# Optimization experiments

Hardware: AMD Instinct MI355X
Metric: run time of the kernel (lower is better)

Reference implementation:

```python
import jax, jax.numpy as jnp
import numpy as np

EPS = 1e-5  # torch nn.LayerNorm default


def _ln(x, g, b):
    m = jnp.mean(x, axis=-1, keepdims=True)
    v = jnp.mean(jnp.square(x - m), axis=-1, keepdims=True)
    return (x - m) * jax.lax.rsqrt(v + EPS) * g + b


def setup_inputs() -> dict:
    key = jax.random.key(0)
    ks = jax.random.split(key, 21)
    B, D, H, O = 32768, 512, 256, 128
    E, T, NS, NT, G = 10, 3, 4, 2, 64

    def rn(k, shape, s=0.02):
        return jax.random.normal(k, shape, jnp.float32) * s

    return dict(
        x=jax.random.normal(ks[0], (B, D), jnp.float32),
        ew1=rn(ks[1], (E, D, H)), eb1=rn(ks[2], (E, H)),
        eg1=1.0 + rn(ks[3], (E, H), 0.1), ebt1=rn(ks[4], (E, H), 0.1),
        ew2=rn(ks[5], (E, H, H)), eb2=rn(ks[6], (E, H)),
        eg2=1.0 + rn(ks[7], (E, H), 0.1), ebt2=rn(ks[8], (E, H), 0.1),
        ew3=rn(ks[9], (E, H, O)), eb3=rn(ks[10], (E, O)),
        eg3=1.0 + rn(ks[11], (E, O), 0.1), ebt3=rn(ks[12], (E, O), 0.1),
        tg_w1=rn(ks[13], (T, D, G)), tg_b1=rn(ks[14], (T, G)),
        tg_w2=rn(ks[15], (T, G, NS + NT)), tg_b2=rn(ks[16], (T, NS + NT)),
        sg_w1=rn(ks[17], (D, G)), sg_b1=rn(ks[18], (G,)),
        sg_w2=rn(ks[19], (G, E)), sg_b2=rn(ks[20], (E,)),
    )


def reference(x, ew1, eb1, eg1, ebt1, ew2, eb2, eg2, ebt2,
              ew3, eb3, eg3, ebt3, tg_w1, tg_b1, tg_w2, tg_b2,
              sg_w1, sg_b1, sg_w2, sg_b2):
    NS, NT, T = 4, 2, 3  # num_shared_experts, num_task_experts, num_tasks
    # Batched expert MLPs (eval mode: dropout is identity). eo: [E, B, O]
    h = jax.nn.relu(_ln(jnp.einsum('bd,edh->ebh', x, ew1) + eb1[:, None, :],
                        eg1[:, None, :], ebt1[:, None, :]))
    h = jax.nn.relu(_ln(jnp.einsum('ebh,ehk->ebk', h, ew2) + eb2[:, None, :],
                        eg2[:, None, :], ebt2[:, None, :]))
    eo = jax.nn.relu(_ln(jnp.einsum('ebh,eho->ebo', h, ew3) + eb3[:, None, :],
                         eg3[:, None, :], ebt3[:, None, :]))
    E, B, O = eo.shape
    shared = eo[:NS]                              # [NS, B, O]
    task_eo = eo[NS:].reshape(T, NT, B, O)        # [T, NT, B, O]

    # Per-task gates: softmax over NS+NT experts. gw: [T, B, NS+NT]
    gh = jax.nn.relu(jnp.einsum('bd,tdg->tbg', x, tg_w1) + tg_b1[:, None, :])
    gw = jax.nn.softmax(jnp.einsum('tbg,tge->tbe', gh, tg_w2) + tg_b2[:, None, :],
                        axis=-1)
    # combined: [T, NS+NT, B, O] (shared first, matching torch.cat order)
    combined = jnp.concatenate(
        [jnp.broadcast_to(shared[None], (T, NS, B, O)), task_eo], axis=1)
    task_out = jnp.einsum('tbe,tebo->tbo', gw, combined)  # [T, B, O]

    # Shared gate over all E experts (order: shared, task0, task1, task2)
    sgh = jax.nn.relu(x @ sg_w1 + sg_b1)
    sgw = jax.nn.softmax(sgh @ sg_w2 + sg_b2, axis=-1)    # [B, E]
    shared_out = jnp.einsum('be,ebo->bo', sgw, eo)        # [B, O]

    # Pack (task_final_outputs list, shared_output) as one [T+1, B, O] array
    return jnp.concatenate([task_out, shared_out[None]], axis=0)
```

## Files before the change

### kernel.cpp

```cpp
#include <hip/hip_runtime.h>
#include <math.h>

typedef __attribute__((ext_vector_type(8))) _Float16 half8;
typedef __attribute__((ext_vector_type(8))) short short8;
typedef __attribute__((ext_vector_type(4))) float float4v;

static __device__ __forceinline__ unsigned short f2h(float f) {
  union { _Float16 h; unsigned short u; } c;
  c.h = (_Float16)f;
  return c.u;
}
static __device__ __forceinline__ float h2f(unsigned short u) {
  union { unsigned short u; _Float16 h; } c;
  c.u = u;
  return (float)c.h;
}

static __device__ __forceinline__ void gload16(const unsigned short* g,
                                               unsigned short* l) {
  __builtin_amdgcn_global_load_lds(
      (const __attribute__((address_space(1))) unsigned int*)g,
      (__attribute__((address_space(3))) unsigned int*)l, 16, 0, 0);
}

__global__ __launch_bounds__(256)
void split_pack(const float* __restrict__ src, unsigned short* __restrict__ dh,
                unsigned short* __restrict__ dl, int K, int N) {
  __shared__ float t[32][33];
  src += (size_t)blockIdx.z * K * N;
  const size_t tsz = (size_t)N * 32;
  const size_t tb = ((size_t)blockIdx.z * (K >> 5) + blockIdx.x) * tsz;
  const int k0 = blockIdx.x * 32, n0 = blockIdx.y * 32;
  const int tid = threadIdx.x;
  const int r = tid >> 3, c4 = (tid & 7) * 4;

  const float4 v = *(const float4*)(src + (size_t)(k0 + r) * N + n0 + c4);
  t[r][c4 + 0] = v.x; t[r][c4 + 1] = v.y; t[r][c4 + 2] = v.z; t[r][c4 + 3] = v.w;
  __syncthreads();

  const int sel = tid >> 7;
  const int rl = (tid >> 2) & 31;
  const int qq = tid & 3;
  short8 vv;
  #pragma unroll
  for (int j = 0; j < 8; ++j) {
    const float f = t[qq * 8 + j][rl];
    const unsigned short hb = f2h(f);
    ((unsigned short*)&vv)[j] = sel ? f2h(f - h2f(hb)) : hb;
  }
  unsigned short* dst = (sel ? dl : dh) + tb +
      (size_t)(n0 + rl) * 32 + (qq ^ ((rl >> 1) & 3)) * 8;
  *(short8*)dst = vv;
}

template<int N, int NT>
__device__ __forceinline__ void ln_store_f16(
    float4v (*acc)[4], int w, int m, int q,
    const float* __restrict__ bias, const float* __restrict__ gamma,
    const float* __restrict__ beta,
    unsigned short* __restrict__ dst, int dstride,
    float (*sumP)[4], float (*sqP)[4]) {
  constexpr int NW = N / 4;
  float cb[NT], cg[NT], cbt[NT];
  #pragma unroll
  for (int t = 0; t < NT; ++t) {
    const int col = w * NW + t * 16 + m;
    cb[t] = bias[col]; cg[t] = gamma[col]; cbt[t] = beta[col];
  }
  #pragma unroll
  for (int s = 0; s < 4; ++s)
    #pragma unroll
    for (int r = 0; r < 4; ++r) {
      float s1 = 0.f, s2 = 0.f;
      #pragma unroll
      for (int t = 0; t < NT; ++t) {
        const float v = acc[s][t][r] + cb[t];
        s1 += v; s2 += v * v;
      }
      #pragma unroll
      for (int off = 1; off < 16; off <<= 1) {
        s1 += __shfl_xor(s1, off, 16);
        s2 += __shfl_xor(s2, off, 16);
      }
      if (m == 0) {
        sumP[s * 16 + q * 4 + r][w] = s1;
        sqP[s * 16 + q * 4 + r][w] = s2;
      }
    }
  __syncthreads();
  #pragma unroll
  for (int s = 0; s < 4; ++s)
    #pragma unroll
    for (int r = 0; r < 4; ++r) {
      const int row = s * 16 + q * 4 + r;
      const float S1 = sumP[row][0] + sumP[row][1] + sumP[row][2] + sumP[row][3];
      const float S2 = sqP[row][0] + sqP[row][1] + sqP[row][2] + sqP[row][3];
      const float mean = S1 * (1.f / N);
      const float var = S2 * (1.f / N) - mean * mean;
      const float inv = rsqrtf(var + 1e-5f);
      #pragma unroll
      for (int t = 0; t < NT; ++t) {
        const float o =
            fmaxf((acc[s][t][r] + cb[t] - mean) * inv * cg[t] + cbt[t], 0.f);
        dst[row * dstride + w * NW + t * 16 + m] = f2h(o);
      }
    }
  __syncthreads();
}

__global__ __launch_bounds__(256, 2)
void expert_tower(const float* __restrict__ x,
                  const unsigned short* __restrict__ w1h,
                  const unsigned short* __restrict__ w1l,
                  const float* __restrict__ eb1, const float* __restrict__ eg1,
                  const float* __restrict__ ebt1,
                  const unsigned short* __restrict__ w2h,
                  const unsigned short* __restrict__ w2l,
                  const float* __restrict__ eb2, const float* __restrict__ eg2,
                  const float* __restrict__ ebt2,
                  const unsigned short* __restrict__ w3h,
                  const unsigned short* __restrict__ w3l,
                  const float* __restrict__ eb3, const float* __restrict__ eg3,
                  const float* __restrict__ ebt3,
                  unsigned short* __restrict__ eo, int B) {
  __shared__ __align__(16) unsigned short pool[40960];
  float (*sumP)[4] = (float (*)[4])(pool + 16384);
  float (*sqP)[4]  = (float (*)[4])(pool + 16896);
  unsigned short* hbuf = pool + 24064;

  const int tid = threadIdx.x;
  const int w = tid >> 6, lane = tid & 63, m = lane & 15, q = lane >> 4;
  const int qs8 = (q ^ ((m >> 1) & 3)) * 8;
  const int wb = w * 512;
  const int m0 = blockIdx.x * 64;
  const int e = blockIdx.y;
  const int arow = tid >> 2, ap = tid & 3;
  const int aswz = arow * 32 + (ap ^ ((arow >> 1) & 3)) * 8;

  eb1 += (size_t)e * 256; eg1 += (size_t)e * 256; ebt1 += (size_t)e * 256;
  eb2 += (size_t)e * 256; eg2 += (size_t)e * 256; ebt2 += (size_t)e * 256;
  eb3 += (size_t)e * 128; eg3 += (size_t)e * 128; ebt3 += (size_t)e * 128;

  float4v acc[4][4];

  #pragma unroll
  for (int s = 0; s < 4; ++s)
    #pragma unroll
    for (int t = 0; t < 4; ++t) acc[s][t] = (float4v){0.f, 0.f, 0.f, 0.f};

  const float* xrow = x + (size_t)(m0 + arow) * 512 + ap * 8;
  float4 f0 = *(const float4*)xrow;
  float4 f1 = *(const float4*)(xrow + 4);

  {
    const float fv[8] = {f0.x, f0.y, f0.z, f0.w, f1.x, f1.y, f1.z, f1.w};
    half8 ra, rla;
    #pragma unroll
    for (int j = 0; j < 8; ++j) {
      const _Float16 hb = (_Float16)fv[j];
      ra[j] = hb;
      rla[j] = (_Float16)(fv[j] - (float)hb);
    }
    *(half8*)(pool + aswz) = ra;
    *(half8*)(pool + 2048 + aswz) = rla;
    const size_t tb = ((size_t)(e * 16)) * 8192 + tid * 8;
    #pragma unroll
    for (int i = 0; i < 4; ++i) {
      gload16(w1h + tb + i * 2048, pool + 8192 + wb + i * 2048);
      gload16(w1l + tb + i * 2048, pool + 8192 + 8192 + wb + i * 2048);
    }
    __builtin_amdgcn_sched_barrier(0);
    f0 = *(const float4*)(xrow + 32);
    f1 = *(const float4*)(xrow + 36);
    __builtin_amdgcn_sched_barrier(0);
    asm volatile("s_waitcnt vmcnt(2) lgkmcnt(0)" ::: "memory");
    __builtin_amdgcn_sched_barrier(0);
    __builtin_amdgcn_s_barrier();
  }

  #pragma unroll 2
  for (int kt = 0; kt < 16; ++kt) {
    const int cur = kt & 1, nxt = cur ^ 1;
    if (kt < 15) {
      const float fv[8] = {f0.x, f0.y, f0.z, f0.w, f1.x, f1.y, f1.z, f1.w};
      half8 ra, rla;
      #pragma unroll
      for (int j = 0; j < 8; ++j) {
        const _Float16 hb = (_Float16)fv[j];
        ra[j] = hb;
        rla[j] = (_Float16)(fv[j] - (float)hb);
      }
      *(half8*)(pool + nxt * 4096 + aswz) = ra;
      *(half8*)(pool + nxt * 4096 + 2048 + aswz) = rla;
      const size_t tb = ((size_t)(e * 16 + kt + 1)) * 8192 + tid * 8;
      #pragma unroll
      for (int i = 0; i < 4; ++i) {
        gload16(w1h + tb + i * 2048, pool + 8192 + nxt * 16384 + wb + i * 2048);
        gload16(w1l + tb + i * 2048,
                pool + 8192 + nxt * 16384 + 8192 + wb + i * 2048);
      }
      __builtin_amdgcn_sched_barrier(0);
      const int ktn = (kt < 14) ? kt + 2 : 15;
      f0 = *(const float4*)(xrow + ktn * 32);
      f1 = *(const float4*)(xrow + ktn * 32 + 4);
      __builtin_amdgcn_sched_barrier(0);
    }
    __builtin_amdgcn_s_setprio(1);
    half8 ah[4], al[4];
    const unsigned short* ab = pool + cur * 4096;
    #pragma unroll
    for (int s = 0; s < 4; ++s) {
      const int off = (s * 16 + m) * 32 + qs8;
      ah[s] = *(const half8*)(ab + off);
      al[s] = *(const half8*)(ab + 2048 + off);
    }
    const unsigned short* bb = pool + 8192 + cur * 16384;
    #pragma unroll
    for (int t = 0; t < 4; ++t) {
      const int boff = (w * 64 + t * 16 + m) * 32 + qs8;
      const half8 bh = *(const half8*)(bb + boff);
      const half8 bl = *(const half8*)(bb + 8192 + boff);
      #pragma unroll
      for (int s = 0; s < 4; ++s) {
        acc[s][t] = __builtin_amdgcn_mfma_f32_16x16x32_f16(ah[s], bh, acc[s][t], 0, 0, 0);
        acc[s][t] = __builtin_amdgcn_mfma_f32_16x16x32_f16(al[s], bh, acc[s][t], 0, 0, 0);
        acc[s][t] = __builtin_amdgcn_mfma_f32_16x16x32_f16(ah[s], bl, acc[s][t], 0, 0, 0);
      }
    }
    __builtin_amdgcn_s_setprio(0);
    if (kt < 15) {
      __builtin_amdgcn_sched_barrier(0);
      asm volatile("s_waitcnt vmcnt(2) lgkmcnt(0)" ::: "memory");
      __builtin_amdgcn_sched_barrier(0);
      __builtin_amdgcn_s_barrier();
    }
  }
  ln_store_f16<256, 4>(acc, w, m, q, eb1, eg1, ebt1, hbuf, 264, sumP, sqP);

  #pragma unroll
  for (int s = 0; s < 4; ++s)
    #pragma unroll
    for (int t = 0; t < 4; ++t) acc[s][t] = (float4v){0.f, 0.f, 0.f, 0.f};

  short8 rh[4], rl[4];
  {
    const size_t tb = ((size_t)(e * 8)) * 8192 + tid * 8;
    #pragma unroll
    for (int i = 0; i < 4; ++i) {
      rh[i] = *(const short8*)(w2h + tb + i * 2048);
      rl[i] = *(const short8*)(w2l + tb + i * 2048);
    }
  }
  for (int kt = 0; kt < 8; ++kt) {
    if (kt) __builtin_amdgcn_s_barrier();
    #pragma unroll
    for (int i = 0; i < 4; ++i) {
      *(short8*)(pool + i * 2048 + tid * 8) = rh[i];
      *(short8*)(pool + 8192 + i * 2048 + tid * 8) = rl[i];
    }
    if (kt < 7) {
      const size_t tb = ((size_t)(e * 8 + kt + 1)) * 8192 + tid * 8;
      #pragma unroll
      for (int i = 0; i < 4; ++i) {
        rh[i] = *(const short8*)(w2h + tb + i * 2048);
        rl[i] = *(const short8*)(w2l + tb + i * 2048);
      }
    }
    __builtin_amdgcn_sched_barrier(0);
    asm volatile("s_waitcnt lgkmcnt(0)" ::: "memory");
    __builtin_amdgcn_sched_barrier(0);
    __builtin_amdgcn_s_barrier();
    __builtin_amdgcn_s_setprio(1);
    half8 ah[4];
    #pragma unroll
    for (int s = 0; s < 4; ++s)
      ah[s] = *(const half8*)(hbuf + (s * 16 + m) * 264 + kt * 32 + q * 8);
    #pragma unroll
    for (int t = 0; t < 4; ++t) {
      const int boff = (w * 64 + t * 16 + m) * 32 + qs8;
      const half8 bh = *(const half8*)(pool + boff);
      const half8 bl = *(const half8*)(pool + 8192 + boff);
      #pragma unroll
      for (int s = 0; s < 4; ++s) {
        acc[s][t] = __builtin_amdgcn_mfma_f32_16x16x32_f16(ah[s], bh, acc[s][t], 0, 0, 0);
        acc[s][t] = __builtin_amdgcn_mfma_f32_16x16x32_f16(ah[s], bl, acc[s][t], 0, 0, 0);
      }
    }
    __builtin_amdgcn_s_setprio(0);
  }
  ln_store_f16<256, 4>(acc, w, m, q, eb2, eg2, ebt2, hbuf, 264, sumP, sqP);

  #pragma unroll
  for (int s = 0; s < 4; ++s)
    #pragma unroll
    for (int t = 0; t < 2; ++t) acc[s][t] = (float4v){0.f, 0.f, 0.f, 0.f};

  short8 sh[2], sl[2];
  {
    const size_t tb = ((size_t)(e * 8)) * 4096 + tid * 8;
    #pragma unroll
    for (int i = 0; i < 2; ++i) {
      sh[i] = *(const short8*)(w3h + tb + i * 2048);
      sl[i] = *(const short8*)(w3l + tb + i * 2048);
    }
  }
  for (int kt = 0; kt < 8; ++kt) {
    if (kt) __builtin_amdgcn_s_barrier();
    #pragma unroll
    for (int i = 0; i < 2; ++i) {
      *(short8*)(pool + i * 2048 + tid * 8) = sh[i];
      *(short8*)(pool + 4096 + i * 2048 + tid * 8) = sl[i];
    }
    if (kt < 7) {
      const size_t tb = ((size_t)(e * 8 + kt + 1)) * 4096 + tid * 8;
      #pragma unroll
      for (int i = 0; i < 2; ++i) {
        sh[i] = *(const short8*)(w3h + tb + i * 2048);
        sl[i] = *(const short8*)(w3l + tb + i * 2048);
      }
    }
    __builtin_amdgcn_sched_barrier(0);
    asm volatile("s_waitcnt lgkmcnt(0)" ::: "memory");
    __builtin_amdgcn_sched_barrier(0);
    __builtin_amdgcn_s_barrier();
    __builtin_amdgcn_s_setprio(1);
    half8 ah[4];
    #pragma unroll
    for (int s = 0; s < 4; ++s)
      ah[s] = *(const half8*)(hbuf + (s * 16 + m) * 264 + kt * 32 + q * 8);
    #pragma unroll
    for (int t = 0; t < 2; ++t) {
      const int boff = (w * 32 + t * 16 + m) * 32 + qs8;
      const half8 bh = *(const half8*)(pool + boff);
      const half8 bl = *(const half8*)(pool + 4096 + boff);
      #pragma unroll
      for (int s = 0; s < 4; ++s) {
        acc[s][t] = __builtin_amdgcn_mfma_f32_16x16x32_f16(ah[s], bh, acc[s][t], 0, 0, 0);
        acc[s][t] = __builtin_amdgcn_mfma_f32_16x16x32_f16(ah[s], bl, acc[s][t], 0, 0, 0);
      }
    }
    __builtin_amdgcn_s_setprio(0);
  }
  unsigned short* rp = pool;
  ln_store_f16<128, 2>(acc, w, m, q, eb3, eg3, ebt3, rp, 136, sumP, sqP);
  #pragma unroll
  for (int i = 0; i < 4; ++i) {
    const int c = tid + i * 256;
    const int rowc = c >> 4, c8 = c & 15;
    *(short8*)(eo + ((size_t)e * B + m0 + rowc) * 128 + c8 * 8) =
        *(const short8*)(rp + rowc * 136 + c8 * 8);
  }
}

template<int NOUT>
__global__ __launch_bounds__(256, 4)
void gate_gemm(const float* __restrict__ x, const unsigned short* __restrict__ twh,
               const unsigned short* __restrict__ twl,
               const float* __restrict__ b1, const float* __restrict__ w2,
               const float* __restrict__ b2, float* __restrict__ outw,
               int slice_base, int B) {
  __shared__ __align__(16) char smem[32768];
  unsigned short* gp = (unsigned short*)smem;
  float (*ghs)[65] = (float (*)[65])smem;
  float* wls = (float*)(smem + 16640);
  float* bls = (float*)(smem + 16640 + 64 * NOUT * 4);

  const int tid = threadIdx.x;
  const int w = tid >> 6, lane = tid & 63, m = lane & 15, q = lane >> 4;
  const int qs8 = (q ^ ((m >> 1) & 3)) * 8;
  const int wb = w * 512;
  const int m0 = blockIdx.x * 64;
  const int sl = blockIdx.y;
  const int slice = slice_base + sl;
  const int arow = tid >> 2, ap = tid & 3;
  const int aswz = arow * 32 + (ap ^ ((arow >> 1) & 3)) * 8;
  const float* bias = b1 + (size_t)sl * 64;
  const float* w2p = w2 + (size_t)sl * 64 * NOUT;
  const float* b2p = b2 + (size_t)sl * NOUT;
  float* outp = outw + (size_t)sl * B * NOUT;

  float4v acc[4];
  #pragma unroll
  for (int s = 0; s < 4; ++s) acc[s] = (float4v){0.f, 0.f, 0.f, 0.f};

  const float* xrow = x + (size_t)(m0 + arow) * 512 + ap * 8;
  float4 f0 = *(const float4*)xrow;
  float4 f1 = *(const float4*)(xrow + 4);

  {
    const float fv[8] = {f0.x, f0.y, f0.z, f0.w, f1.x, f1.y, f1.z, f1.w};
    half8 ra, rla;
    #pragma unroll
    for (int j = 0; j < 8; ++j) {
      const _Float16 hb = (_Float16)fv[j];
      ra[j] = hb;
      rla[j] = (_Float16)(fv[j] - (float)hb);
    }
    *(half8*)(gp + aswz) = ra;
    *(half8*)(gp + 2048 + aswz) = rla;
    const size_t tb = ((size_t)(slice * 16)) * 2048 + tid * 8;
    gload16(twh + tb, gp + 8192 + wb);
    gload16(twl + tb, gp + 8192 + 2048 + wb);
    __builtin_amdgcn_sched_barrier(0);
    f0 = *(const float4*)(xrow + 32);
    f1 = *(const float4*)(xrow + 36);
    __builtin_amdgcn_sched_barrier(0);
    asm volatile("s_waitcnt vmcnt(2) lgkmcnt(0)" ::: "memory");
    __builtin_amdgcn_sched_barrier(0);
    __builtin_amdgcn_s_barrier();
  }

  #pragma unroll 2
  for (int kt = 0; kt < 16; ++kt) {
    const int cur = kt & 1, nxt = cur ^ 1;
    if (kt < 15) {
      const float fv[8] = {f0.x, f0.y, f0.z, f0.w, f1.x, f1.y, f1.z, f1.w};
      half8 ra, rla;
      #pragma unroll
      for (int j = 0; j < 8; ++j) {
        const _Float16 hb = (_Float16)fv[j];
        ra[j] = hb;
        rla[j] = (_Float16)(fv[j] - (float)hb);
      }
      *(half8*)(gp + nxt * 4096 + aswz) = ra;
      *(half8*)(gp + nxt * 4096 + 2048 + aswz) = rla;
      const size_t tb = ((size_t)(slice * 16 + kt + 1)) * 2048 + tid * 8;
      gload16(twh + tb, gp + 8192 + nxt * 4096 + wb);
      gload16(twl + tb, gp + 8192 + nxt * 4096 + 2048 + wb);
      __builtin_amdgcn_sched_barrier(0);
      const int ktn = (kt < 14) ? kt + 2 : 15;
      f0 = *(const float4*)(xrow + ktn * 32);
      f1 = *(const float4*)(xrow + ktn * 32 + 4);
      __builtin_amdgcn_sched_barrier(0);
    }
    __builtin_amdgcn_s_setprio(1);
    const unsigned short* ab = gp + cur * 4096;
    const unsigned short* bb = gp + 8192 + cur * 4096;
    const int boff = (w * 16 + m) * 32 + qs8;
    const half8 bh = *(const half8*)(bb + boff);
    const half8 bl = *(const half8*)(bb + 2048 + boff);
    #pragma unroll
    for (int s = 0; s < 4; ++s) {
      const int aoff = (s * 16 + m) * 32 + qs8;
      const half8 ah = *(const half8*)(ab + aoff);
      const half8 al = *(const half8*)(ab + 2048 + aoff);
      acc[s] = __builtin_amdgcn_mfma_f32_16x16x32_f16(ah, bh, acc[s], 0, 0, 0);
      acc[s] = __builtin_amdgcn_mfma_f32_16x16x32_f16(al, bh, acc[s], 0, 0, 0);
      acc[s] = __builtin_amdgcn_mfma_f32_16x16x32_f16(ah, bl, acc[s], 0, 0, 0);
    }
    __builtin_amdgcn_s_setprio(0);
    if (kt < 15) {
      __builtin_amdgcn_sched_barrier(0);
      asm volatile("s_waitcnt vmcnt(2) lgkmcnt(0)" ::: "memory");
      __builtin_amdgcn_sched_barrier(0);
      __builtin_amdgcn_s_barrier();
    }
  }

  const float cb = bias[w * 16 + m];
  __syncthreads();
  #pragma unroll
  for (int s = 0; s < 4; ++s)
    #pragma unroll
    for (int r = 0; r < 4; ++r)
      ghs[s * 16 + q * 4 + r][w * 16 + m] = fmaxf(acc[s][r] + cb, 0.f);
  for (int f = tid; f < 64 * NOUT; f += 256) wls[f] = w2p[f];
  if (tid < NOUT) bls[tid] = b2p[tid];
  __syncthreads();

  if (tid < 64) {
    float a[NOUT];
    #pragma unroll
    for (int n = 0; n < NOUT; ++n) a[n] = bls[n];
    for (int k = 0; k < 64; ++k) {
      const float g = ghs[tid][k];
      #pragma unroll
      for (int n = 0; n < NOUT; ++n) a[n] = fmaf(g, wls[k * NOUT + n], a[n]);
    }
    float mx = a[0];
    #pragma unroll
    for (int n = 1; n < NOUT; ++n) mx = fmaxf(mx, a[n]);
    float sum = 0.f;
    #pragma unroll
    for (int n = 0; n < NOUT; ++n) { a[n] = expf(a[n] - mx); sum += a[n]; }
    const float r = 1.f / sum;
    #pragma unroll
    for (int n = 0; n < NOUT; ++n)
      outp[(size_t)(m0 + tid) * NOUT + n] = a[n] * r;
  }
}

__global__ __launch_bounds__(256)
void combine(const unsigned short* __restrict__ eo, const float* __restrict__ gw,
             const float* __restrict__ sgw, float* __restrict__ out, int B) {
  const int tid = threadIdx.x;
  const int gb = blockIdx.x * 16 + (tid >> 4);
  const int c0 = (tid & 15) * 8;

  float a[4][8];
  #pragma unroll
  for (int s = 0; s < 4; ++s)
    #pragma unroll
    for (int i = 0; i < 8; ++i) a[s][i] = 0.f;

  #pragma unroll
  for (int e = 0; e < 10; ++e) {
    const half8 vv = *(const half8*)(eo + ((size_t)e * B + gb) * 128 + c0);
    float f[8];
    #pragma unroll
    for (int i = 0; i < 8; ++i) f[i] = (float)vv[i];
    float c[4];
    c[3] = sgw[(size_t)gb * 10 + e];
    c[0] = c[1] = c[2] = 0.f;
    if (e < 4) {
      c[0] = gw[((size_t)0 * B + gb) * 6 + e];
      c[1] = gw[((size_t)1 * B + gb) * 6 + e];
      c[2] = gw[((size_t)2 * B + gb) * 6 + e];
    } else {
      const int tt = (e - 4) >> 1;
      c[tt] = gw[((size_t)tt * B + gb) * 6 + 4 + ((e - 4) & 1)];
    }
    #pragma unroll
    for (int s = 0; s < 4; ++s)
      #pragma unroll
      for (int i = 0; i < 8; ++i) a[s][i] = fmaf(c[s], f[i], a[s][i]);
  }

  #pragma unroll
  for (int s = 0; s < 4; ++s) {
    float* p = out + ((size_t)s * B + gb) * 128 + c0;
    const float4 v0 = {a[s][0], a[s][1], a[s][2], a[s][3]};
    const float4 v1 = {a[s][4], a[s][5], a[s][6], a[s][7]};
    *(float4*)p = v0;
    *(float4*)(p + 4) = v1;
  }
}

extern "C" void kernel_launch(void* const* d_in, const int* in_sizes, int n_in,
                              void* d_out, int out_size, void* d_ws, size_t ws_size,
                              hipStream_t stream) {
  const float* x     = (const float*)d_in[0];
  const float* ew1   = (const float*)d_in[1];
  const float* eb1   = (const float*)d_in[2];
  const float* eg1   = (const float*)d_in[3];
  const float* ebt1  = (const float*)d_in[4];
  const float* ew2   = (const float*)d_in[5];
  const float* eb2   = (const float*)d_in[6];
  const float* eg2   = (const float*)d_in[7];
  const float* ebt2  = (const float*)d_in[8];
  const float* ew3   = (const float*)d_in[9];
  const float* eb3   = (const float*)d_in[10];
  const float* eg3   = (const float*)d_in[11];
  const float* ebt3  = (const float*)d_in[12];
  const float* tg_w1 = (const float*)d_in[13];
  const float* tg_b1 = (const float*)d_in[14];
  const float* tg_w2 = (const float*)d_in[15];
  const float* tg_b2 = (const float*)d_in[16];
  const float* sg_w1 = (const float*)d_in[17];
  const float* sg_b1 = (const float*)d_in[18];
  const float* sg_w2 = (const float*)d_in[19];
  const float* sg_b2 = (const float*)d_in[20];
  float* out = (float*)d_out;

  const int B = 32768, D = 512, H = 256, O = 128, G = 64, E = 10;
  (void)D; (void)H; (void)O; (void)G;

  char* p = (char*)d_ws;
  unsigned short* w1h  = (unsigned short*)p; p += (size_t)E * 16 * 8192 * 2;
  unsigned short* w1l  = (unsigned short*)p; p += (size_t)E * 16 * 8192 * 2;
  unsigned short* w2h  = (unsigned short*)p; p += (size_t)E * 8 * 8192 * 2;
  unsigned short* w2l  = (unsigned short*)p; p += (size_t)E * 8 * 8192 * 2;
  unsigned short* w3h  = (unsigned short*)p; p += (size_t)E * 8 * 4096 * 2;
  unsigned short* w3l  = (unsigned short*)p; p += (size_t)E * 8 * 4096 * 2;
  unsigned short* twh  = (unsigned short*)p; p += (size_t)4 * 16 * 2048 * 2;
  unsigned short* twl  = (unsigned short*)p; p += (size_t)4 * 16 * 2048 * 2;
  float* gwb  = (float*)p; p += (size_t)3 * B * 6 * 4;
  float* sgwb = (float*)p; p += (size_t)B * 10 * 4;
  unsigned short* eo = (unsigned short*)p;

  split_pack<<<dim3(16, 8, E), 256, 0, stream>>>(ew1, w1h, w1l, 512, 256);
  split_pack<<<dim3(8, 8, E), 256, 0, stream>>>(ew2, w2h, w2l, 256, 256);
  split_pack<<<dim3(8, 4, E), 256, 0, stream>>>(ew3, w3h, w3l, 256, 128);
  split_pack<<<dim3(16, 2, 3), 256, 0, stream>>>(tg_w1, twh, twl, 512, 64);
  split_pack<<<dim3(16, 2, 1), 256, 0, stream>>>(
      sg_w1, twh + (size_t)3 * 16 * 2048, twl + (size_t)3 * 16 * 2048, 512, 64);

  gate_gemm<6><<<dim3(B / 64, 3), 256, 0, stream>>>(
      x, twh, twl, tg_b1, tg_w2, tg_b2, gwb, 0, B);
  gate_gemm<10><<<dim3(B / 64, 1), 256, 0, stream>>>(
      x, twh, twl, sg_b1, sg_w2, sg_b2, sgwb, 3, B);

  expert_tower<<<dim3(B / 64, E), 256, 0, stream>>>(
      x, w1h, w1l, eb1, eg1, ebt1, w2h, w2l, eb2, eg2, ebt2,
      w3h, w3l, eb3, eg3, ebt3, eo, B);

  combine<<<B / 16, 256, 0, stream>>>(eo, gwb, sgwb, out, B);
}
```

Measured before the change: 725.5 us.

## Fuse gate GEMMs into expert tower kernel as an extra grid slice

Removes the separate gate_gemm launches and treats the four gate first-layer weight matrices (3 task gates + shared gate, 64 columns each) as a 256-wide pseudo-expert handled by blockIdx.y==0 of the main tower kernel. A new pack kernel interleaves the gate weights into the same tiled layout as expert layer 1, so the existing first GEMM loop is reused. Each wave then runs its own gate's second layer and softmax. This saves two kernel launches and a second read of x. The gate blocks exit early, which may leave the grid unbalanced.

```diff
diff --git a/kernel.cpp b/kernel.cpp
--- a/kernel.cpp
+++ b/kernel.cpp
@@ -53,6 +53,40 @@
   *(short8*)dst = vv;
 }
 
+__global__ __launch_bounds__(256)
+void split_pack_gate(const float* __restrict__ tg_w1,
+                     const float* __restrict__ sg_w1,
+                     unsigned short* __restrict__ dh,
+                     unsigned short* __restrict__ dl) {
+  __shared__ float t[32][33];
+  const int slice = blockIdx.z;
+  const float* src = (slice < 3) ? tg_w1 + (size_t)slice * 512 * 64 : sg_w1;
+  const int k0 = blockIdx.x * 32, n0 = blockIdx.y * 32;
+  const size_t tb = ((size_t)blockIdx.x * 4 + slice) * 2048;
+  const int tid = threadIdx.x;
+  const int r = tid >> 3, c4 = (tid & 7) * 4;
+
+  if (c4 < 32) {
+    const float4 v = *(const float4*)(src + (size_t)(k0 + r) * 64 + n0 + c4);
+    t[r][c4 + 0] = v.x; t[r][c4 + 1] = v.y; t[r][c4 + 2] = v.z; t[r][c4 + 3] = v.w;
+  }
+  __syncthreads();
+
+  const int sel = tid >> 7;
+  const int rl = (tid >> 2) & 31;
+  const int qq = tid & 3;
+  short8 vv;
+  #pragma unroll
+  for (int j = 0; j < 8; ++j) {
+    const float f = t[qq * 8 + j][rl];
+    const unsigned short hb = f2h(f);
+    ((unsigned short*)&vv)[j] = sel ? f2h(f - h2f(hb)) : hb;
+  }
+  unsigned short* dst = (sel ? dl : dh) + tb +
+      (size_t)(n0 + rl) * 32 + (qq ^ ((rl >> 1) & 3)) * 8;
+  *(short8*)dst = vv;
+}
+
 template<int N, int NT>
 __device__ __forceinline__ void ln_store_f16(
     float4v (*acc)[4], int w, int m, int q,
@@ -108,21 +142,50 @@
   __syncthreads();
 }
 
+template<int NOUT>
+static __device__ __forceinline__ void gate2_row(
+    const float* __restrict__ ghs_row, const float* __restrict__ wls,
+    const float* __restrict__ b2p, float* __restrict__ outp) {
+  float a[NOUT];
+  #pragma unroll
+  for (int n = 0; n < NOUT; ++n) a[n] = b2p[n];
+  for (int k = 0; k < 64; ++k) {
+    const float g = ghs_row[k];
+    #pragma unroll
+    for (int n = 0; n < NOUT; ++n) a[n] = fmaf(g, wls[k * NOUT + n], a[n]);
+  }
+  float mx = a[0];
+  #pragma unroll
+  for (int n = 1; n < NOUT; ++n) mx = fmaxf(mx, a[n]);
+  float sum = 0.f;
+  #pragma unroll
+  for (int n = 0; n < NOUT; ++n) { a[n] = expf(a[n] - mx); sum += a[n]; }
+  const float r = 1.f / sum;
+  #pragma unroll
+  for (int n = 0; n < NOUT; ++n) outp[n] = a[n] * r;
+}
+
 __global__ __launch_bounds__(256, 2)
-void expert_tower(const float* __restrict__ x,
-                  const unsigned short* __restrict__ w1h,
-                  const unsigned short* __restrict__ w1l,
-                  const float* __restrict__ eb1, const float* __restrict__ eg1,
-                  const float* __restrict__ ebt1,
-                  const unsigned short* __restrict__ w2h,
-                  const unsigned short* __restrict__ w2l,
-                  const float* __restrict__ eb2, const float* __restrict__ eg2,
-                  const float* __restrict__ ebt2,
-                  const unsigned short* __restrict__ w3h,
-                  const unsigned short* __restrict__ w3l,
-                  const float* __restrict__ eb3, const float* __restrict__ eg3,
-                  const float* __restrict__ ebt3,
-                  unsigned short* __restrict__ eo, int B) {
+void fused_main(const float* __restrict__ x,
+                const unsigned short* __restrict__ w1h,
+                const unsigned short* __restrict__ w1l,
+                const float* __restrict__ eb1, const float* __restrict__ eg1,
+                const float* __restrict__ ebt1,
+                const unsigned short* __restrict__ w2h,
+                const unsigned short* __restrict__ w2l,
+                const float* __restrict__ eb2, const float* __restrict__ eg2,
+                const float* __restrict__ ebt2,
+                const unsigned short* __restrict__ w3h,
+                const unsigned short* __restrict__ w3l,
+                const float* __restrict__ eb3, const float* __restrict__ eg3,
+                const float* __restrict__ ebt3,
+                const unsigned short* __restrict__ twh,
+                const unsigned short* __restrict__ twl,
+                const float* __restrict__ tg_b1, const float* __restrict__ sg_b1,
+                const float* __restrict__ tg_w2, const float* __restrict__ tg_b2,
+                const float* __restrict__ sg_w2, const float* __restrict__ sg_b2,
+                float* __restrict__ gwb, float* __restrict__ sgwb,
+                unsigned short* __restrict__ eo, int B) {
   __shared__ __align__(16) unsigned short pool[40960];
   float (*sumP)[4] = (float (*)[4])(pool + 16384);
   float (*sqP)[4]  = (float (*)[4])(pool + 16896);
@@ -133,13 +196,15 @@
   const int qs8 = (q ^ ((m >> 1) & 3)) * 8;
   const int wb = w * 512;
   const int m0 = blockIdx.x * 64;
-  const int e = blockIdx.y;
+  const int y = blockIdx.y;
+  const bool is_gate = (y == 0);
+  const int e = y - 1;
   const int arow = tid >> 2, ap = tid & 3;
   const int aswz = arow * 32 + (ap ^ ((arow >> 1) & 3)) * 8;
 
-  eb1 += (size_t)e * 256; eg1 += (size_t)e * 256; ebt1 += (size_t)e * 256;
-  eb2 += (size_t)e * 256; eg2 += (size_t)e * 256; ebt2 += (size_t)e * 256;
-  eb3 += (size_t)e * 128; eg3 += (size_t)e * 128; ebt3 += (size_t)e * 128;
+  const unsigned short* p1h = is_gate ? twh : w1h;
+  const unsigned short* p1l = is_gate ? twl : w1l;
+  const size_t p1base = is_gate ? 0 : (size_t)e * 16;
 
   float4v acc[4][4];
 
@@ -163,11 +228,11 @@
     }
     *(half8*)(pool + aswz) = ra;
     *(half8*)(pool + 2048 + aswz) = rla;
-    const size_t tb = ((size_t)(e * 16)) * 8192 + tid * 8;
+    const size_t tb = p1base * 8192 + tid * 8;
     #pragma unroll
     for (int i = 0; i < 4; ++i) {
-      gload16(w1h + tb + i * 2048, pool + 8192 + wb + i * 2048);
-      gload16(w1l + tb + i * 2048, pool + 8192 + 8192 + wb + i * 2048);
+      gload16(p1h + tb + i * 2048, pool + 8192 + wb + i * 2048);
+      gload16(p1l + tb + i * 2048, pool + 8192 + 8192 + wb + i * 2048);
     }
     __builtin_amdgcn_sched_barrier(0);
     f0 = *(const float4*)(xrow + 32);
@@ -192,11 +257,11 @@
       }
       *(half8*)(pool + nxt * 4096 + aswz) = ra;
       *(half8*)(pool + nxt * 4096 + 2048 + aswz) = rla;
-      const size_t tb = ((size_t)(e * 16 + kt + 1)) * 8192 + tid * 8;
+      const size_t tb = (p1base + kt + 1) * 8192 + tid * 8;
       #pragma unroll
       for (int i = 0; i < 4; ++i) {
-        gload16(w1h + tb + i * 2048, pool + 8192 + nxt * 16384 + wb + i * 2048);
-        gload16(w1l + tb + i * 2048,
+        gload16(p1h + tb + i * 2048, pool + 8192 + nxt * 16384 + wb + i * 2048);
+        gload16(p1l + tb + i * 2048,
                 pool + 8192 + nxt * 16384 + 8192 + wb + i * 2048);
       }
       __builtin_amdgcn_sched_barrier(0);
@@ -235,7 +300,47 @@
       __builtin_amdgcn_s_barrier();
     }
   }
-  ln_store_f16<256, 4>(acc, w, m, q, eb1, eg1, ebt1, hbuf, 264, sumP, sqP);
+
+  if (is_gate) {
+    __syncthreads();
+    float* ghs = (float*)pool + (size_t)w * 64 * 65;
+    float* wls = (float*)((char*)pool + 66560 + (size_t)w * 2560);
+    const float* b1p = (w < 3) ? tg_b1 + (size_t)w * 64 : sg_b1;
+    const float* w2p = (w < 3) ? tg_w2 + (size_t)w * 64 * 6 : sg_w2;
+    const float* b2p = (w < 3) ? tg_b2 + (size_t)w * 6 : sg_b2;
+    const int nout = (w < 3) ? 6 : 10;
+    float cb[4];
+    #pragma unroll
+    for (int t = 0; t < 4; ++t) cb[t] = b1p[t * 16 + m];
+    #pragma unroll
+    for (int s = 0; s < 4; ++s)
+      #pragma unroll
+      for (int t = 0; t < 4; ++t)
+        #pragma unroll
+        for (int r = 0; r < 4; ++r)
+          ghs[(s * 16 + q * 4 + r) * 65 + t * 16 + m] =
+              fmaxf(acc[s][t][r] + cb[t], 0.f);
+    for (int f = lane; f < 64 * nout; f += 64) wls[f] = w2p[f];
+    const int row = lane;
+    if (w < 3)
+      gate2_row<6>(ghs + row * 65, wls, b2p,
+                   gwb + ((size_t)w * B + m0 + row) * 6);
+    else
+      gate2_row<10>(ghs + row * 65, wls, b2p, sgwb + (size_t)(m0 + row) * 10);
+    return;
+  }
+
+  const float* geb1 = eb1 + (size_t)e * 256;
+  const float* geg1 = eg1 + (size_t)e * 256;
+  const float* gebt1 = ebt1 + (size_t)e * 256;
+  const float* geb2 = eb2 + (size_t)e * 256;
+  const float* geg2 = eg2 + (size_t)e * 256;
+  const float* gebt2 = ebt2 + (size_t)e * 256;
+  const float* geb3 = eb3 + (size_t)e * 128;
+  const float* geg3 = eg3 + (size_t)e * 128;
+  const float* gebt3 = ebt3 + (size_t)e * 128;
+
+  ln_store_f16<256, 4>(acc, w, m, q, geb1, geg1, gebt1, hbuf, 264, sumP, sqP);
 
   #pragma unroll
   for (int s = 0; s < 4; ++s)
@@ -288,7 +393,7 @@
     }
     __builtin_amdgcn_s_setprio(0);
   }
-  ln_store_f16<256, 4>(acc, w, m, q, eb2, eg2, ebt2, hbuf, 264, sumP, sqP);
+  ln_store_f16<256, 4>(acc, w, m, q, geb2, geg2, gebt2, hbuf, 264, sumP, sqP);
 
   #pragma unroll
   for (int s = 0; s < 4; ++s)
@@ -342,151 +447,13 @@
     __builtin_amdgcn_s_setprio(0);
   }
   unsigned short* rp = pool;
-  ln_store_f16<128, 2>(acc, w, m, q, eb3, eg3, ebt3, rp, 136, sumP, sqP);
+  ln_store_f16<128, 2>(acc, w, m, q, geb3, geg3, gebt3, rp, 136, sumP, sqP);
   #pragma unroll
   for (int i = 0; i < 4; ++i) {
     const int c = tid + i * 256;
     const int rowc = c >> 4, c8 = c & 15;
     *(short8*)(eo + ((size_t)e * B + m0 + rowc) * 128 + c8 * 8) =
         *(const short8*)(rp + rowc * 136 + c8 * 8);
-  }
-}
-
-template<int NOUT>
-__global__ __launch_bounds__(256, 4)
-void gate_gemm(const float* __restrict__ x, const unsigned short* __restrict__ twh,
-               const unsigned short* __restrict__ twl,
-               const float* __restrict__ b1, const float* __restrict__ w2,
-               const float* __restrict__ b2, float* __restrict__ outw,
-               int slice_base, int B) {
-  __shared__ __align__(16) char smem[32768];
-  unsigned short* gp = (unsigned short*)smem;
-  float (*ghs)[65] = (float (*)[65])smem;
-  float* wls = (float*)(smem + 16640);
-  float* bls = (float*)(smem + 16640 + 64 * NOUT * 4);
-
-  const int tid = threadIdx.x;
-  const int w = tid >> 6, lane = tid & 63, m = lane & 15, q = lane >> 4;
-  const int qs8 = (q ^ ((m >> 1) & 3)) * 8;
-  const int wb = w * 512;
-  const int m0 = blockIdx.x * 64;
-  const int sl = blockIdx.y;
-  const int slice = slice_base + sl;
-  const int arow = tid >> 2, ap = tid & 3;
-  const int aswz = arow * 32 + (ap ^ ((arow >> 1) & 3)) * 8;
-  const float* bias = b1 + (size_t)sl * 64;
-  const float* w2p = w2 + (size_t)sl * 64 * NOUT;
-  const float* b2p = b2 + (size_t)sl * NOUT;
-  float* outp = outw + (size_t)sl * B * NOUT;
-
-  float4v acc[4];
-  #pragma unroll
-  for (int s = 0; s < 4; ++s) acc[s] = (float4v){0.f, 0.f, 0.f, 0.f};
-
-  const float* xrow = x + (size_t)(m0 + arow) * 512 + ap * 8;
-  float4 f0 = *(const float4*)xrow;
-  float4 f1 = *(const float4*)(xrow + 4);
-
-  {
-    const float fv[8] = {f0.x, f0.y, f0.z, f0.w, f1.x, f1.y, f1.z, f1.w};
-    half8 ra, rla;
-    #pragma unroll
-    for (int j = 0; j < 8; ++j) {
-      const _Float16 hb = (_Float16)fv[j];
-      ra[j] = hb;
-      rla[j] = (_Float16)(fv[j] - (float)hb);
-    }
-    *(half8*)(gp + aswz) = ra;
-    *(half8*)(gp + 2048 + aswz) = rla;
-    const size_t tb = ((size_t)(slice * 16)) * 2048 + tid * 8;
-    gload16(twh + tb, gp + 8192 + wb);
-    gload16(twl + tb, gp + 8192 + 2048 + wb);
-    __builtin_amdgcn_sched_barrier(0);
-    f0 = *(const float4*)(xrow + 32);
-    f1 = *(const float4*)(xrow + 36);
-    __builtin_amdgcn_sched_barrier(0);
-    asm volatile("s_waitcnt vmcnt(2) lgkmcnt(0)" ::: "memory");
-    __builtin_amdgcn_sched_barrier(0);
-    __builtin_amdgcn_s_barrier();
-  }
-
-  #pragma unroll 2
-  for (int kt = 0; kt < 16; ++kt) {
-    const int cur = kt & 1, nxt = cur ^ 1;
-    if (kt < 15) {
-      const float fv[8] = {f0.x, f0.y, f0.z, f0.w, f1.x, f1.y, f1.z, f1.w};
-      half8 ra, rla;
-      #pragma unroll
-      for (int j = 0; j < 8; ++j) {
-        const _Float16 hb = (_Float16)fv[j];
-        ra[j] = hb;
-        rla[j] = (_Float16)(fv[j] - (float)hb);
-      }
-      *(half8*)(gp + nxt * 4096 + aswz) = ra;
-      *(half8*)(gp + nxt * 4096 + 2048 + aswz) = rla;
-      const size_t tb = ((size_t)(slice * 16 + kt + 1)) * 2048 + tid * 8;
-      gload16(twh + tb, gp + 8192 + nxt * 4096 + wb);
-      gload16(twl + tb, gp + 8192 + nxt * 4096 + 2048 + wb);
-      __builtin_amdgcn_sched_barrier(0);
-      const int ktn = (kt < 14) ? kt + 2 : 15;
-      f0 = *(const float4*)(xrow + ktn * 32);
-      f1 = *(const float4*)(xrow + ktn * 32 + 4);
-      __builtin_amdgcn_sched_barrier(0);
-    }
-    __builtin_amdgcn_s_setprio(1);
-    const unsigned short* ab = gp + cur * 4096;
-    const unsigned short* bb = gp + 8192 + cur * 4096;
-    const int boff = (w * 16 + m) * 32 + qs8;
-    const half8 bh = *(const half8*)(bb + boff);
-    const half8 bl = *(const half8*)(bb + 2048 + boff);
-    #pragma unroll
-    for (int s = 0; s < 4; ++s) {
-      const int aoff = (s * 16 + m) * 32 + qs8;
-      const half8 ah = *(const half8*)(ab + aoff);
-      const half8 al = *(const half8*)(ab + 2048 + aoff);
-      acc[s] = __builtin_amdgcn_mfma_f32_16x16x32_f16(ah, bh, acc[s], 0, 0, 0);
-      acc[s] = __builtin_amdgcn_mfma_f32_16x16x32_f16(al, bh, acc[s], 0, 0, 0);
-      acc[s] = __builtin_amdgcn_mfma_f32_16x16x32_f16(ah, bl, acc[s], 0, 0, 0);
-    }
-    __builtin_amdgcn_s_setprio(0);
-    if (kt < 15) {
-      __builtin_amdgcn_sched_barrier(0);
-      asm volatile("s_waitcnt vmcnt(2) lgkmcnt(0)" ::: "memory");
-      __builtin_amdgcn_sched_barrier(0);
-      __builtin_amdgcn_s_barrier();
-    }
-  }
-
-  const float cb = bias[w * 16 + m];
-  __syncthreads();
-  #pragma unroll
-  for (int s = 0; s < 4; ++s)
-    #pragma unroll
-    for (int r = 0; r < 4; ++r)
-      ghs[s * 16 + q * 4 + r][w * 16 + m] = fmaxf(acc[s][r] + cb, 0.f);
-  for (int f = tid; f < 64 * NOUT; f += 256) wls[f] = w2p[f];
-  if (tid < NOUT) bls[tid] = b2p[tid];
-  __syncthreads();
-
-  if (tid < 64) {
-    float a[NOUT];
-    #pragma unroll
-    for (int n = 0; n < NOUT; ++n) a[n] = bls[n];
-    for (int k = 0; k < 64; ++k) {
-      const float g = ghs[tid][k];
-      #pragma unroll
-      for (int n = 0; n < NOUT; ++n) a[n] = fmaf(g, wls[k * NOUT + n], a[n]);
-    }
-    float mx = a[0];
-    #pragma unroll
-    for (int n = 1; n < NOUT; ++n) mx = fmaxf(mx, a[n]);
-    float sum = 0.f;
-    #pragma unroll
-    for (int n = 0; n < NOUT; ++n) { a[n] = expf(a[n] - mx); sum += a[n]; }
-    const float r = 1.f / sum;
-    #pragma unroll
-    for (int n = 0; n < NOUT; ++n)
-      outp[(size_t)(m0 + tid) * NOUT + n] = a[n] * r;
   }
 }
 
@@ -572,8 +539,8 @@
   unsigned short* w2l  = (unsigned short*)p; p += (size_t)E * 8 * 8192 * 2;
   unsigned short* w3h  = (unsigned short*)p; p += (size_t)E * 8 * 4096 * 2;
   unsigned short* w3l  = (unsigned short*)p; p += (size_t)E * 8 * 4096 * 2;
-  unsigned short* twh  = (unsigned short*)p; p += (size_t)4 * 16 * 2048 * 2;
-  unsigned short* twl  = (unsigned short*)p; p += (size_t)4 * 16 * 2048 * 2;
+  unsigned short* twh  = (unsigned short*)p; p += (size_t)16 * 8192 * 2;
+  unsigned short* twl  = (unsigned short*)p; p += (size_t)16 * 8192 * 2;
   float* gwb  = (float*)p; p += (size_t)3 * B * 6 * 4;
   float* sgwb = (float*)p; p += (size_t)B * 10 * 4;
   unsigned short* eo = (unsigned short*)p;
@@ -581,18 +548,13 @@
   split_pack<<<dim3(16, 8, E), 256, 0, stream>>>(ew1, w1h, w1l, 512, 256);
   split_pack<<<dim3(8, 8, E), 256, 0, stream>>>(ew2, w2h, w2l, 256, 256);
   split_pack<<<dim3(8, 4, E), 256, 0, stream>>>(ew3, w3h, w3l, 256, 128);
-  split_pack<<<dim3(16, 2, 3), 256, 0, stream>>>(tg_w1, twh, twl, 512, 64);
-  split_pack<<<dim3(16, 2, 1), 256, 0, stream>>>(
-      sg_w1, twh + (size_t)3 * 16 * 2048, twl + (size_t)3 * 16 * 2048, 512, 64);
-
-  gate_gemm<6><<<dim3(B / 64, 3), 256, 0, stream>>>(
-      x, twh, twl, tg_b1, tg_w2, tg_b2, gwb, 0, B);
-  gate_gemm<10><<<dim3(B / 64, 1), 256, 0, stream>>>(
-      x, twh, twl, sg_b1, sg_w2, sg_b2, sgwb, 3, B);
-
-  expert_tower<<<dim3(B / 64, E), 256, 0, stream>>>(
+  split_pack_gate<<<dim3(16, 2, 4), 256, 0, stream>>>(tg_w1, sg_w1, twh, twl);
+
+  fused_main<<<dim3(B / 64, 11), 256, 0, stream>>>(
       x, w1h, w1l, eb1, eg1, ebt1, w2h, w2l, eb2, eg2, ebt2,
-      w3h, w3l, eb3, eg3, ebt3, eo, B);
+      w3h, w3l, eb3, eg3, ebt3,
+      twh, twl, tg_b1, sg_b1, tg_w2, tg_b2, sg_w2, sg_b2,
+      gwb, sgwb, eo, B);
 
   combine<<<B / 16, 256, 0, stream>>>(eo, gwb, sgwb, out, B);
 }
```

New measurement: 738.4 us. Within noise of the previous version (+1.8%).
